# Optimization experiments

Measured on AMD Instinct MI355X. Metric: run time of the kernel, lower is better.

Reference implementation:

```python
import jax, jax.numpy as jnp
import numpy as np
from jax import lax

BIG = jnp.float32(1e10)  # initial 'infinite' min-distance


def farthest_point_sampling(points, nsamples):
    """Exact iterative FPS. points: (B, P, 3) -> indices (B, nsamples) int32.

    The KD-tree partitioning in QuickFPS is an acceleration structure; the
    reference math is the canonical running-min-distance / argmax FPS.
    """
    B, P, _ = points.shape

    def step(carry, _):
        min_d, last_idx = carry
        # (B, 1, 3) coordinates of the most recently selected point
        last_pt = jnp.take_along_axis(points, last_idx[:, None, None], axis=1)
        d = jnp.sum((points - last_pt) ** 2, axis=-1)  # (B, P)
        min_d = jnp.minimum(min_d, d)
        nxt = jnp.argmax(min_d, axis=-1).astype(jnp.int32)  # (B,)
        return (min_d, nxt), nxt

    init_idx = jnp.zeros((B,), jnp.int32)  # CUDA FPS starts from point 0
    init_d = jnp.full((B, P), BIG, dtype=points.dtype)
    (_, _), rest = lax.scan(step, (init_d, init_idx), None, length=nsamples - 1)
    # rest: (nsamples-1, B) -> (B, nsamples)
    indices = jnp.concatenate([init_idx[None, :], rest], axis=0).T
    return indices


def setup_inputs() -> dict:
    key = jax.random.key(0)
    points = jax.random.normal(key, (32, 65536, 3), dtype=jnp.float32)
    return {"points": points}


def reference(points):
    nsamples = 1024
    indices = farthest_point_sampling(points, nsamples)  # (B, nsamples)
    # gather_points: (B, nsamples, 3)
    sampled_points = jnp.take_along_axis(points, indices[:, :, None], axis=1)
    return indices, sampled_points
```

## Files before the change

kernel.cpp:

```cpp
#include <hip/hip_runtime.h>

#define NB 32
#define NP 65536
#define NS 1024
#define NT 1024
#define BPB 8
#define CHUNK (NP / BPB)
#define PPT2 (CHUNK / NT)

typedef unsigned long long u64;
typedef unsigned int u32;
typedef int int4v __attribute__((ext_vector_type(4)));

__global__ __launch_bounds__(NT) void fps_v7(const float* __restrict__ pts,
                                             float* __restrict__ out,
                                             u32* __restrict__ slots) {
#pragma clang fp contract(off)
    const int bid = blockIdx.x;
    const int b = bid >> 3;
    const int j = bid & 7;
    const int t = threadIdx.x;
    const int base = j * CHUNK;
    const float* __restrict__ pb = pts + (size_t)b * NP * 3;
    float* __restrict__ out_idx = out + (size_t)b * NS;
    float* __restrict__ out_pts = out + (size_t)NB * NS + (size_t)b * NS * 3;
    u32* __restrict__ slot_b = slots + (size_t)b * NS * BPB * 8;

    __shared__ float P[CHUNK * 3];
    __shared__ u64 cand[NT / 64];
    __shared__ int sel_hist[NS];
    __shared__ float qsh[3];

    {
        const float4* __restrict__ src4 = (const float4*)(pb + (size_t)base * 3);
        float4* dst4 = (float4*)P;
#pragma unroll
        for (int k = 0; k < (CHUNK * 3 / 4) / NT; ++k) dst4[t + k * NT] = src4[t + k * NT];
    }

    if (t == 0) {
        sel_hist[0] = 0;
        if (j == 0) out_idx[0] = 0.0f;
        qsh[0] = pb[0]; qsh[1] = pb[1]; qsh[2] = pb[2];
    }
    __syncthreads();

    float px[PPT2], py[PPT2], pz[PPT2], md[PPT2];
#pragma unroll
    for (int i = 0; i < PPT2; ++i) {
        const int li = t + i * NT;
        px[i] = P[li * 3 + 0];
        py[i] = P[li * 3 + 1];
        pz[i] = P[li * 3 + 2];
        md[i] = 1e10f;
    }

    float qx = qsh[0], qy = qsh[1], qz = qsh[2];

    const int wave = t >> 6;
    const int lane = t & 63;

    for (int s = 1; s < NS; ++s) {
        float bestv = -1.0f;
        int besti = 0;
#pragma unroll
        for (int i = 0; i < PPT2; ++i) {
            float dx = px[i] - qx;
            float dy = py[i] - qy;
            float dz = pz[i] - qz;
            float d = (dx * dx + dy * dy) + dz * dz;
            float nmd = fminf(md[i], d);
            md[i] = nmd;
            if (nmd > bestv) { bestv = nmd; besti = t + i * NT; }
        }
        u64 pk = ((u64)__float_as_uint(bestv) << 32) |
                 (u64)(0xFFFFFFFFu - (u32)(base + besti));
#pragma unroll
        for (int m = 32; m >= 1; m >>= 1) {
            u64 o = __shfl_xor(pk, m, 64);
            pk = (o > pk) ? o : pk;
        }
        if (lane == 0) cand[wave] = pk;
        __syncthreads();
        if (wave == 0) {
            u64 c = cand[lane & 15];
#pragma unroll
            for (int m = 8; m >= 1; m >>= 1) {
                u64 o = __shfl_xor(c, m, 64);
                c = (o > c) ? o : c;
            }
            const int g0 = (int)(0xFFFFFFFFu - (u32)(c & 0xFFFFFFFFull));
            float wx0 = 0.f, wy0 = 0.f, wz0 = 0.f;
            if (lane == 0) {
                const int lw = g0 - base;
                wx0 = P[lw * 3 + 0];
                wy0 = P[lw * 3 + 1];
                wz0 = P[lw * 3 + 2];
                int4v h0, h1;
                h0.x = (int)(u32)(c & 0xFFFFFFFFull);
                h0.y = (int)(u32)(c >> 32);
                h0.z = __float_as_int(wx0);
                h0.w = __float_as_int(wy0);
                h1.x = h0.x;
                h1.y = h0.y;
                h1.z = __float_as_int(wz0);
                h1.w = 0;
                u32* sp = slot_b + ((size_t)s * BPB + j) * 8;
                asm volatile(
                    "global_store_dwordx4 %0, %2, off sc0 sc1\n\t"
                    "global_store_dwordx4 %1, %3, off sc0 sc1"
                    :: "v"(sp), "v"(sp + 4), "v"(h0), "v"(h1) : "memory");
            }
            if (lane < BPB) {
                u64 k = 0;
                float wx = 0.f, wy = 0.f, wz = 0.f;
                if (lane != j) {
                    const u32* pp = slot_b + ((size_t)s * BPB + lane) * 8;
                    int4v a, bb;
                    for (;;) {
                        asm volatile(
                            "global_load_dwordx4 %0, %2, off sc0 sc1\n\t"
                            "global_load_dwordx4 %1, %3, off sc0 sc1\n\t"
                            "s_waitcnt vmcnt(0)"
                            : "=&v"(a), "=&v"(bb)
                            : "v"(pp), "v"(pp + 4) : "memory");
                        if (a.x != 0 && a.x == bb.x && a.y == bb.y) break;
                    }
                    k = ((u64)(u32)a.y << 32) | (u32)a.x;
                    wx = __int_as_float(a.z);
                    wy = __int_as_float(a.w);
                    wz = __int_as_float(bb.z);
                }
                u64 mx = (c > k) ? c : k;
#pragma unroll
                for (int m = 4; m >= 1; m >>= 1) {
                    u64 o = __shfl_xor(mx, m, 64);
                    mx = (o > mx) ? o : mx;
                }
                const int g = (int)(0xFFFFFFFFu - (u32)(mx & 0xFFFFFFFFull));
                const int jw = (g >> 13) & 7;
                float sx = __shfl(wx, jw, 64);
                float sy = __shfl(wy, jw, 64);
                float sz = __shfl(wz, jw, 64);
                if (lane == 0) {
                    sel_hist[s] = g;
                    if (jw == j) { qsh[0] = wx0; qsh[1] = wy0; qsh[2] = wz0; }
                    else         { qsh[0] = sx;  qsh[1] = sy;  qsh[2] = sz;  }
                    if (j == 0) out_idx[s] = (float)g;
                }
            }
        }
        __syncthreads();
        qx = qsh[0]; qy = qsh[1]; qz = qsh[2];
    }

    if (j == 0) {
        const int gi = sel_hist[t];
        const float* __restrict__ p = pb + (size_t)gi * 3;
        out_pts[(size_t)t * 3 + 0] = p[0];
        out_pts[(size_t)t * 3 + 1] = p[1];
        out_pts[(size_t)t * 3 + 2] = p[2];
    }
}

__global__ __launch_bounds__(NT) void fps_slots(const float* __restrict__ pts,
                                                float* __restrict__ out,
                                                u64* __restrict__ slots) {
#pragma clang fp contract(off)
    const int bid = blockIdx.x;
    const int b = bid >> 3;
    const int j = bid & 7;
    const int t = threadIdx.x;
    const int base = j * CHUNK;
    const float* __restrict__ pb = pts + (size_t)b * NP * 3;
    float* __restrict__ out_idx = out + (size_t)b * NS;
    float* __restrict__ out_pts = out + (size_t)NB * NS + (size_t)b * NS * 3;
    u64* __restrict__ slot_b = slots + (size_t)b * NS * BPB;

    __shared__ float P[CHUNK * 3];
    __shared__ u64 cand[NT / 64];
    __shared__ int sel_hist[NS];
    __shared__ float qsh[3];

    {
        const float4* __restrict__ src4 = (const float4*)(pb + (size_t)base * 3);
        float4* dst4 = (float4*)P;
#pragma unroll
        for (int k = 0; k < (CHUNK * 3 / 4) / NT; ++k) dst4[t + k * NT] = src4[t + k * NT];
    }
    float md[PPT2];
#pragma unroll
    for (int i = 0; i < PPT2; ++i) md[i] = 1e10f;
    if (t == 0) {
        sel_hist[0] = 0;
        if (j == 0) out_idx[0] = 0.0f;
        qsh[0] = pb[0]; qsh[1] = pb[1]; qsh[2] = pb[2];
    }
    __syncthreads();
    float qx = qsh[0], qy = qsh[1], qz = qsh[2];
    const int wave = t >> 6;
    const int lane = t & 63;
    for (int s = 1; s < NS; ++s) {
        float bestv = -1.0f;
        int besti = 0;
#pragma unroll
        for (int i = 0; i < PPT2; ++i) {
            const int li = t + i * NT;
            const float* __restrict__ p = P + li * 3;
            float dx = p[0] - qx, dy = p[1] - qy, dz = p[2] - qz;
            float d = (dx * dx + dy * dy) + dz * dz;
            float nmd = fminf(md[i], d);
            md[i] = nmd;
            if (nmd > bestv) { bestv = nmd; besti = li; }
        }
        u64 pk = ((u64)__float_as_uint(bestv) << 32) |
                 (u64)(0xFFFFFFFFu - (u32)(base + besti));
#pragma unroll
        for (int m = 32; m >= 1; m >>= 1) {
            u64 o = __shfl_xor(pk, m, 64);
            pk = (o > pk) ? o : pk;
        }
        if (lane == 0) cand[wave] = pk;
        __syncthreads();
        if (wave == 0) {
            u64 c = (lane < 16) ? cand[lane] : 0ull;
#pragma unroll
            for (int m = 8; m >= 1; m >>= 1) {
                u64 o = __shfl_xor(c, m, 64);
                c = (o > c) ? o : c;
            }
            if (lane == 0) {
                __hip_atomic_store(&slot_b[(size_t)s * BPB + j], c,
                                   __ATOMIC_RELAXED, __HIP_MEMORY_SCOPE_AGENT);
            }
            u64 x = 0;
            if (lane < BPB) {
                const u64* sp = &slot_b[(size_t)s * BPB + lane];
                while ((x = __hip_atomic_load(sp, __ATOMIC_RELAXED,
                                              __HIP_MEMORY_SCOPE_AGENT)) == 0ull) {
                    __builtin_amdgcn_s_sleep(1);
                }
            }
#pragma unroll
            for (int m = 4; m >= 1; m >>= 1) {
                u64 o = __shfl_xor(x, m, 64);
                x = (o > x) ? o : x;
            }
            if (lane == 0) {
                int w = (int)(0xFFFFFFFFu - (u32)(x & 0xFFFFFFFFull));
                sel_hist[s] = w;
                const float* __restrict__ q = pb + (size_t)w * 3;
                qsh[0] = q[0]; qsh[1] = q[1]; qsh[2] = q[2];
                if (j == 0) out_idx[s] = (float)w;
            }
        }
        __syncthreads();
        qx = qsh[0]; qy = qsh[1]; qz = qsh[2];
    }
    if (j == 0) {
        const int gi = sel_hist[t];
        const float* __restrict__ p = pb + (size_t)gi * 3;
        out_pts[(size_t)t * 3 + 0] = p[0];
        out_pts[(size_t)t * 3 + 1] = p[1];
        out_pts[(size_t)t * 3 + 2] = p[2];
    }
}

extern "C" void kernel_launch(void* const* d_in, const int* in_sizes, int n_in,
                              void* d_out, int out_size, void* d_ws, size_t ws_size,
                              hipStream_t stream) {
    const float* pts = (const float*)d_in[0];
    float* out = (float*)d_out;
    (void)in_sizes; (void)n_in; (void)out_size;

    const size_t v7_bytes = (size_t)NB * NS * BPB * 32;
    const size_t slot_bytes = (size_t)NB * NS * BPB * sizeof(u64);
    if (ws_size >= v7_bytes) {
        u32* slots = (u32*)d_ws;
        hipMemsetAsync(d_ws, 0, v7_bytes, stream);
        void* args[] = {(void*)&pts, (void*)&out, (void*)&slots};
        hipLaunchCooperativeKernel((const void*)fps_v7, dim3(NB * BPB), dim3(NT),
                                   args, 0, stream);
    } else {
        u64* slots = (u64*)d_ws;
        hipMemsetAsync(d_ws, 0, slot_bytes, stream);
        void* args[] = {(void*)&pts, (void*)&out, (void*)&slots};
        hipLaunchCooperativeKernel((const void*)fps_slots, dim3(NB * BPB), dim3(NT),
                                   args, 0, stream);
    }
}
```

Measured before the change: 2.222 ms.

## Add L2-coherent fast polling path and float-max wave reduction to FPS

Cross-block exchange slots are now tagged with the step number, and each slot is written twice: once system-coherent (sc0 sc1) and once with sc0 only. Readers first poll with the cheaper sc0 loads for a bounded number of attempts, and fall back to the system-coherent loop after repeated misses. The intra-wave argmax now uses a float max plus ballot and first-set-bit instead of 64-bit packed shuffles, and block-to-batch mapping and per-thread point assignment are reordered. The aim is lower inter-block synchronization latency per step, at the cost of extra stores and reliance on cache-coherence behaviour for correctness.

```diff
diff --git a/kernel.cpp b/kernel.cpp
--- a/kernel.cpp
+++ b/kernel.cpp
@@ -6,20 +6,24 @@
 #define NT 1024
 #define BPB 8
 #define CHUNK (NP / BPB)
-#define PPT2 (CHUNK / NT)
+#define PPT (CHUNK / NT)
+#define FAST_ATT 24
+#define DEMOTE_AFTER 2
 
 typedef unsigned long long u64;
 typedef unsigned int u32;
 typedef int int4v __attribute__((ext_vector_type(4)));
 
-__global__ __launch_bounds__(NT) void fps_v7(const float* __restrict__ pts,
-                                             float* __restrict__ out,
-                                             u32* __restrict__ slots) {
+__global__ __launch_bounds__(NT) void fps_v10(const float* __restrict__ pts,
+                                              float* __restrict__ out,
+                                              u32* __restrict__ slots) {
 #pragma clang fp contract(off)
     const int bid = blockIdx.x;
-    const int b = bid >> 3;
-    const int j = bid & 7;
+    const int b = bid & 31;
+    const int j = bid >> 5;
     const int t = threadIdx.x;
+    const int wave = t >> 6;
+    const int lane = t & 63;
     const int base = j * CHUNK;
     const float* __restrict__ pb = pts + (size_t)b * NP * 3;
     float* __restrict__ out_idx = out + (size_t)b * NS;
@@ -37,7 +41,6 @@
 #pragma unroll
         for (int k = 0; k < (CHUNK * 3 / 4) / NT; ++k) dst4[t + k * NT] = src4[t + k * NT];
     }
-
     if (t == 0) {
         sel_hist[0] = 0;
         if (j == 0) out_idx[0] = 0.0f;
@@ -45,48 +48,47 @@
     }
     __syncthreads();
 
-    float px[PPT2], py[PPT2], pz[PPT2], md[PPT2];
-#pragma unroll
-    for (int i = 0; i < PPT2; ++i) {
-        const int li = t + i * NT;
+    float px[PPT], py[PPT], pz[PPT], md[PPT];
+#pragma unroll
+    for (int i = 0; i < PPT; ++i) {
+        const int li = t * PPT + i;
         px[i] = P[li * 3 + 0];
         py[i] = P[li * 3 + 1];
         pz[i] = P[li * 3 + 2];
         md[i] = 1e10f;
     }
-
     float qx = qsh[0], qy = qsh[1], qz = qsh[2];
 
-    const int wave = t >> 6;
-    const int lane = t & 63;
+    int usefast = 1, fastfail = 0;
 
     for (int s = 1; s < NS; ++s) {
-        float bestv = -1.0f;
-        int besti = 0;
-#pragma unroll
-        for (int i = 0; i < PPT2; ++i) {
+        float bv = -1.0f;
+        int bi = 0;
+#pragma unroll
+        for (int i = 0; i < PPT; ++i) {
             float dx = px[i] - qx;
             float dy = py[i] - qy;
             float dz = pz[i] - qz;
             float d = (dx * dx + dy * dy) + dz * dz;
             float nmd = fminf(md[i], d);
             md[i] = nmd;
-            if (nmd > bestv) { bestv = nmd; besti = t + i * NT; }
-        }
-        u64 pk = ((u64)__float_as_uint(bestv) << 32) |
-                 (u64)(0xFFFFFFFFu - (u32)(base + besti));
-#pragma unroll
-        for (int m = 32; m >= 1; m >>= 1) {
-            u64 o = __shfl_xor(pk, m, 64);
-            pk = (o > pk) ? o : pk;
-        }
-        if (lane == 0) cand[wave] = pk;
+            if (nmd > bv) { bv = nmd; bi = t * PPT + i; }
+        }
+        float m = bv;
+#pragma unroll
+        for (int d1 = 32; d1 >= 1; d1 >>= 1) m = fmaxf(m, __shfl_xor(m, d1, 64));
+        u64 msk = __ballot(bv == m);
+        int src = __ffsll((unsigned long long)msk) - 1;
+        int biw = __shfl(bi, src, 64);
+        if (lane == 0)
+            cand[wave] = ((u64)__float_as_uint(m) << 32) |
+                         (u64)(0xFFFFFFFFu - (u32)(base + biw));
         __syncthreads();
         if (wave == 0) {
             u64 c = cand[lane & 15];
 #pragma unroll
-            for (int m = 8; m >= 1; m >>= 1) {
-                u64 o = __shfl_xor(c, m, 64);
+            for (int d1 = 8; d1 >= 1; d1 >>= 1) {
+                u64 o = __shfl_xor(c, d1, 64);
                 c = (o > c) ? o : c;
             }
             const int g0 = (int)(0xFFFFFFFFu - (u32)(c & 0xFFFFFFFFull));
@@ -97,47 +99,64 @@
                 wy0 = P[lw * 3 + 1];
                 wz0 = P[lw * 3 + 2];
                 int4v h0, h1;
-                h0.x = (int)(u32)(c & 0xFFFFFFFFull);
+                h0.x = s;
                 h0.y = (int)(u32)(c >> 32);
-                h0.z = __float_as_int(wx0);
-                h0.w = __float_as_int(wy0);
-                h1.x = h0.x;
-                h1.y = h0.y;
+                h0.z = (int)(u32)c;
+                h0.w = __float_as_int(wx0);
+                h1.x = s;
+                h1.y = __float_as_int(wy0);
                 h1.z = __float_as_int(wz0);
                 h1.w = 0;
                 u32* sp = slot_b + ((size_t)s * BPB + j) * 8;
                 asm volatile(
                     "global_store_dwordx4 %0, %2, off sc0 sc1\n\t"
-                    "global_store_dwordx4 %1, %3, off sc0 sc1"
+                    "global_store_dwordx4 %1, %3, off sc0 sc1\n\t"
+                    "global_store_dwordx4 %0, %2, off sc0\n\t"
+                    "global_store_dwordx4 %1, %3, off sc0"
                     :: "v"(sp), "v"(sp + 4), "v"(h0), "v"(h1) : "memory");
             }
             if (lane < BPB) {
-                u64 k = 0;
+                u64 k = c;
                 float wx = 0.f, wy = 0.f, wz = 0.f;
                 if (lane != j) {
-                    const u32* pp = slot_b + ((size_t)s * BPB + lane) * 8;
+                    const u32* sp = slot_b + ((size_t)s * BPB + lane) * 8;
                     int4v a, bb;
-                    for (;;) {
-                        asm volatile(
-                            "global_load_dwordx4 %0, %2, off sc0 sc1\n\t"
-                            "global_load_dwordx4 %1, %3, off sc0 sc1\n\t"
-                            "s_waitcnt vmcnt(0)"
-                            : "=&v"(a), "=&v"(bb)
-                            : "v"(pp), "v"(pp + 4) : "memory");
-                        if (a.x != 0 && a.x == bb.x && a.y == bb.y) break;
+                    int got = 0;
+                    if (usefast) {
+                        for (int it = 0; it < FAST_ATT && !got; ++it) {
+                            asm volatile(
+                                "global_load_dwordx4 %0, %2, off sc0\n\t"
+                                "global_load_dwordx4 %1, %3, off sc0\n\t"
+                                "s_waitcnt vmcnt(0)"
+                                : "=&v"(a), "=&v"(bb)
+                                : "v"(sp), "v"(sp + 4) : "memory");
+                            got = (a.x == s && bb.x == s);
+                        }
+                        if (got) fastfail = 0;
+                        else if (++fastfail >= DEMOTE_AFTER) usefast = 0;
                     }
-                    k = ((u64)(u32)a.y << 32) | (u32)a.x;
-                    wx = __int_as_float(a.z);
-                    wy = __int_as_float(a.w);
+                    if (!got) {
+                        for (;;) {
+                            asm volatile(
+                                "global_load_dwordx4 %0, %2, off sc0 sc1\n\t"
+                                "global_load_dwordx4 %1, %3, off sc0 sc1\n\t"
+                                "s_waitcnt vmcnt(0)"
+                                : "=&v"(a), "=&v"(bb)
+                                : "v"(sp), "v"(sp + 4) : "memory");
+                            if (a.x == s && bb.x == s) break;
+                        }
+                    }
+                    k = ((u64)(u32)a.y << 32) | (u32)a.z;
+                    wx = __int_as_float(a.w);
+                    wy = __int_as_float(bb.y);
                     wz = __int_as_float(bb.z);
                 }
-                u64 mx = (c > k) ? c : k;
-#pragma unroll
-                for (int m = 4; m >= 1; m >>= 1) {
-                    u64 o = __shfl_xor(mx, m, 64);
-                    mx = (o > mx) ? o : mx;
+#pragma unroll
+                for (int d1 = 4; d1 >= 1; d1 >>= 1) {
+                    u64 o = __shfl_xor(k, d1, 64);
+                    k = (o > k) ? o : k;
                 }
-                const int g = (int)(0xFFFFFFFFu - (u32)(mx & 0xFFFFFFFFull));
+                const int g = (int)(0xFFFFFFFFu - (u32)(k & 0xFFFFFFFFull));
                 const int jw = (g >> 13) & 7;
                 float sx = __shfl(wx, jw, 64);
                 float sy = __shfl(wy, jw, 64);
@@ -188,9 +207,9 @@
 #pragma unroll
         for (int k = 0; k < (CHUNK * 3 / 4) / NT; ++k) dst4[t + k * NT] = src4[t + k * NT];
     }
-    float md[PPT2];
-#pragma unroll
-    for (int i = 0; i < PPT2; ++i) md[i] = 1e10f;
+    float md[PPT];
+#pragma unroll
+    for (int i = 0; i < PPT; ++i) md[i] = 1e10f;
     if (t == 0) {
         sel_hist[0] = 0;
         if (j == 0) out_idx[0] = 0.0f;
@@ -204,7 +223,7 @@
         float bestv = -1.0f;
         int besti = 0;
 #pragma unroll
-        for (int i = 0; i < PPT2; ++i) {
+        for (int i = 0; i < PPT; ++i) {
             const int li = t + i * NT;
             const float* __restrict__ p = P + li * 3;
             float dx = p[0] - qx, dy = p[1] - qy, dz = p[2] - qz;
@@ -273,13 +292,13 @@
     float* out = (float*)d_out;
     (void)in_sizes; (void)n_in; (void)out_size;
 
-    const size_t v7_bytes = (size_t)NB * NS * BPB * 32;
+    const size_t v10_bytes = (size_t)NB * NS * BPB * 32;
     const size_t slot_bytes = (size_t)NB * NS * BPB * sizeof(u64);
-    if (ws_size >= v7_bytes) {
+    if (ws_size >= v10_bytes) {
         u32* slots = (u32*)d_ws;
-        hipMemsetAsync(d_ws, 0, v7_bytes, stream);
+        hipMemsetAsync(d_ws, 0, v10_bytes, stream);
         void* args[] = {(void*)&pts, (void*)&out, (void*)&slots};
-        hipLaunchCooperativeKernel((const void*)fps_v7, dim3(NB * BPB), dim3(NT),
+        hipLaunchCooperativeKernel((const void*)fps_v10, dim3(NB * BPB), dim3(NT),
                                    args, 0, stream);
     } else {
         u64* slots = (u64*)d_ws;
```

Measured after the change: 3.403 ms. 1.53x slower.
